# Performance work log

Measured on AMD Instinct MI355X. Metric: run time of the kernel, lower is better.

The kernel has to match this reference:

```python
import jax, jax.numpy as jnp
import numpy as np

K, B, T, EH, DH, F = 32, 256, 32, 128, 128, 1


def _p(key, shape, scale=0.1):
    return scale * jax.random.normal(key, shape, jnp.float32)


def setup_inputs() -> dict:
    key = jax.random.key(0)
    ks = jax.random.split(key, 24)
    inp = {
        'input_encoded': jax.random.normal(ks[0], (B, T, EH), jnp.float32),
        'y_prev': jax.random.normal(ks[1], (B, T), jnp.float32),
        'eps': jax.random.normal(ks[2], (T, K, B, DH), jnp.float32),
        'gumbel': jax.random.gumbel(ks[3], (T, B, K, K), jnp.float32),
        # attn_layer: Linear(2*DH+EH -> EH), Tanh, Linear(EH -> 1)
        'attn_W1': _p(ks[4], (2 * DH + EH, EH)),
        'attn_b1': _p(ks[5], (EH,)),
        'attn_W2': _p(ks[6], (EH, 1)),
        'attn_b2': _p(ks[7], (1,)),
        # LSTM(input_size=F, hidden_size=DH); gate order i,f,g,o
        'W_ih': _p(ks[8], (F, 4 * DH)),
        'W_hh': _p(ks[9], (DH, 4 * DH)),
        'b_ih': _p(ks[10], (4 * DH,)),
        'b_hh': _p(ks[11], (4 * DH,)),
        # fc: Linear(EH+F -> F), weights initialized normal_() in torch
        'fc_W': jax.random.normal(ks[12], (EH + F, F), jnp.float32),
        'fc_b': _p(ks[13], (F,)),
        # fc_decoder_final: Linear(DH -> F)
        'fcdec_W': _p(ks[14], (DH, F)),
        'fcdec_b': _p(ks[15], (F,)),
        # fc_encoder_final (passed-in module, modeled as Linear(EH -> F))
        'fcenc_W': _p(ks[16], (EH, F)),
        'fcenc_b': _p(ks[17], (F,)),
        # var_layer: Linear(DH+F -> DH); pdf_layer: Linear(DH+F -> 1)
        'var_W': _p(ks[18], (DH + F, DH)),
        'var_b': _p(ks[19], (DH,)),
        'pdf_W': _p(ks[20], (DH + F, 1)),
        'pdf_b': _p(ks[21], (1,)),
    }
    return inp


def _decoder_fwd(input_encoded, y_prev, eps, gumbel, attn_W1, attn_b1, attn_W2,
                 attn_b2, W_ih, W_hh, b_ih, b_hh, fc_W, fc_b, fcdec_W, fcdec_b,
                 fcenc_W, fcenc_b, var_W, var_b, pdf_W, pdf_b):
    Bn, Tn, EHn = input_encoded.shape
    Kn = eps.shape[1]
    DHn = W_hh.shape[0]

    def lstm_cell(x, h, c):  # x:[N,F], h/c:[N,DH]
        g = x @ W_ih + h @ W_hh + (b_ih + b_hh)
        i, f, gg, o = jnp.split(g, 4, axis=-1)
        c2 = jax.nn.sigmoid(f) * c + jax.nn.sigmoid(i) * jnp.tanh(gg)
        h2 = jax.nn.sigmoid(o) * jnp.tanh(c2)
        return h2, c2

    def step(carry, inp):
        hiddens, cells, _ = carry          # [K,B,DH] particle-major
        yprev_t, eps_t, g_t = inp          # [B], [K,B,DH], [B,K,K]
        hbar = hiddens.mean(axis=0)        # [B,DH]
        cbar = cells.mean(axis=0)
        # attention over all T encoder states
        x = jnp.concatenate([
            jnp.broadcast_to(hbar[:, None, :], (Bn, Tn, DHn)),
            jnp.broadcast_to(cbar[:, None, :], (Bn, Tn, DHn)),
            input_encoded], axis=2)                       # [B,T,2DH+EH]
        a = jnp.tanh(x @ attn_W1 + attn_b1) @ attn_W2 + attn_b2  # [B,T,1]
        beta = jax.nn.softmax(a[..., 0], axis=1)                 # [B,T]
        context = jnp.einsum('bt,bte->be', beta, input_encoded)  # [B,EH]
        y_tilde = jnp.concatenate([context, yprev_t[:, None]], axis=1) @ fc_W + fc_b  # [B,F]
        var = jnp.concatenate([y_tilde, hbar], axis=1) @ var_W + var_b  # [B,DH]
        # one LSTM step for all particles (same input, per-particle state)
        xin = jnp.broadcast_to(y_tilde[None], (Kn, Bn, y_tilde.shape[1])).reshape(Kn * Bn, -1)
        h2, c2 = lstm_cell(xin, hiddens.reshape(Kn * Bn, DHn), cells.reshape(Kn * Bn, DHn))
        h2 = h2.reshape(Kn, Bn, DHn)
        c2 = c2.reshape(Kn, Bn, DHn)
        # reparameterize: mu + eps * softplus(var)
        h2 = h2 + eps_t * jax.nn.softplus(var)[None]
        # sort particles per batch by scalar projection (only hiddens sorted)
        proj = (h2.reshape(-1, DHn) @ fcdec_W + fcdec_b).reshape(Kn, Bn)  # [K,B]
        order = jnp.argsort(proj, axis=0)                                  # [K,B]
        h2 = jnp.take_along_axis(h2, order[:, :, None], axis=0)
        # particle weights; replicate torch's view(-1, K) normalization exactly
        y = jnp.concatenate([h2.reshape(-1, DHn), jnp.tile(y_tilde, (Kn, 1))], axis=1)
        logpdf = (y @ pdf_W + pdf_b)[:, 0]          # [K*B] particle-major flat
        p = jnp.exp(logpdf).reshape(Bn, Kn)         # torch view(-1, K, 1)
        p = p / p.sum(axis=1, keepdims=True)
        w = p.reshape(Kn, Bn).T                     # [B,K]: torch view(K,-1).T
        # multinomial with replacement via gumbel-max (row-normalization implicit)
        idx = jnp.argmax(jnp.log(w + 1e-30)[:, None, :] + g_t, axis=-1)  # [B,K]
        sel = idx.T                                  # [K,B]: new[p,b] = old[idx[b,p], b]
        h2 = jnp.take_along_axis(h2, sel[:, :, None], axis=0)
        c2 = jnp.take_along_axis(c2, sel[:, :, None], axis=0)
        return (h2, c2, context), None

    h0 = jnp.zeros((Kn, Bn, DHn), input_encoded.dtype)
    ctx0 = jnp.zeros((Bn, EHn), input_encoded.dtype)
    (hK, cK, context), _ = jax.lax.scan(step, (h0, h0, ctx0), (y_prev.T, eps, gumbel))
    y_decoder_pred = hK.mean(axis=0) @ fcdec_W + fcdec_b   # [B,F]
    y_encoder_pred = context @ fcenc_W + fcenc_b           # [B,F]
    return y_decoder_pred + y_encoder_pred


def reference(input_encoded, y_prev, eps, gumbel, attn_W1, attn_b1, attn_W2,
              attn_b2, W_ih, W_hh, b_ih, b_hh, fc_W, fc_b, fcdec_W, fcdec_b,
              fcenc_W, fcenc_b, var_W, var_b, pdf_W, pdf_b):
    return _decoder_fwd(input_encoded, y_prev, eps, gumbel, attn_W1, attn_b1,
                        attn_W2, attn_b2, W_ih, W_hh, b_ih, b_hh, fc_W, fc_b,
                        fcdec_W, fcdec_b, fcenc_W, fcenc_b, var_W, var_b,
                        pdf_W, pdf_b)
```

## Files before the change

kernel.cpp:

```cpp
#include <hip/hip_runtime.h>

#define KP 32
#define BN 256
#define TN 32
#define ROWS (KP*BN)
#define NTHR 512

__global__ void k_pre(const float* __restrict__ enc, const float* __restrict__ W1,
                      const float* __restrict__ Whh, const float* __restrict__ Wih,
                      const float* __restrict__ bih, const float* __restrict__ bhh,
                      float* __restrict__ encp, float* __restrict__ Wre,
                      float* __restrict__ wihre, float* __restrict__ bre,
                      unsigned* __restrict__ flags) {
    int bt = blockIdx.x;
    int e  = threadIdx.x;
    __shared__ float row[128];
    row[e] = enc[bt * 128 + e];
    __syncthreads();
    float acc = 0.f;
#pragma unroll 8
    for (int c = 0; c < 128; ++c)
        acc = fmaf(row[c], W1[(256 + c) * 128 + e], acc);
    encp[bt * 128 + e] = acc;

    if (bt < 128) {
        int i = bt * 128 + e;
        int dd = i >> 7, d0 = i & 127;
        float4 v;
        v.x = Whh[dd * 512 + 0 * 128 + d0];
        v.y = Whh[dd * 512 + 1 * 128 + d0];
        v.z = Whh[dd * 512 + 2 * 128 + d0];
        v.w = Whh[dd * 512 + 3 * 128 + d0];
        ((float4*)Wre)[i] = v;
        if (i < 128) {
            float4 a;
            a.x = Wih[0 * 128 + d0]; a.y = Wih[1 * 128 + d0];
            a.z = Wih[2 * 128 + d0]; a.w = Wih[3 * 128 + d0];
            ((float4*)wihre)[d0] = a;
            float4 bb;
            bb.x = bih[0 * 128 + d0] + bhh[0 * 128 + d0];
            bb.y = bih[1 * 128 + d0] + bhh[1 * 128 + d0];
            bb.z = bih[2 * 128 + d0] + bhh[2 * 128 + d0];
            bb.w = bih[3 * 128 + d0] + bhh[3 * 128 + d0];
            ((float4*)bre)[d0] = bb;
        }
    } else if (bt < 192) {
        flags[(bt - 128) * 128 + e] = 0u;
    }
}

struct SharedS {
    float h[KP * 128], c[KP * 128], h2[KP * 128], c2[KP * 128];
    float hb[128], cb[128], hcp[128], red[128];
    float aa[32], beta[32];
    float vsp[128], ctx[128];
    float proj[32], qv[32];
    float pp[32][2], qq[32][2];
    int ord[32], hjo[32], cjo[32];
    float lw[32];
    float yts;
};

__global__ __launch_bounds__(NTHR, 2)
void k_persist(const float* __restrict__ enc, const float* __restrict__ yprev,
               const float* __restrict__ eps, const float* __restrict__ gum,
               const float* __restrict__ W1, const float* __restrict__ b1,
               const float* __restrict__ W2, const float* __restrict__ b2v,
               const float* __restrict__ fcW, const float* __restrict__ fcb,
               const float* __restrict__ fdW, const float* __restrict__ fdb,
               const float* __restrict__ feW, const float* __restrict__ feb,
               const float* __restrict__ varW, const float* __restrict__ varb,
               const float* __restrict__ pdW, const float* __restrict__ pdb,
               const float* __restrict__ encp, const float* __restrict__ Wre,
               const float* __restrict__ wihre, const float* __restrict__ bre,
               float* __restrict__ esg, unsigned* __restrict__ flags,
               float* __restrict__ out) {
    __shared__ SharedS sh;
    const int tid = threadIdx.x;
    const int b   = blockIdx.x;
    const int m   = b >> 5;

    const int w_  = tid >> 6, c0_ = tid & 63;
    const int wr_ = w_ & 3, dh_ = w_ >> 2;
    const int d0_ = dh_ * 64 + c0_;

#pragma unroll
    for (int i = 0; i < 2; ++i) {
        ((float4*)sh.h)[tid + NTHR * i] = make_float4(0.f, 0.f, 0.f, 0.f);
        ((float4*)sh.c)[tid + NTHR * i] = make_float4(0.f, 0.f, 0.f, 0.f);
    }
    __syncthreads();

    for (int t = 0; t < TN; ++t) {
        float epr[8];
        {
            const float* ep = eps + (size_t)t * ROWS * 128
                            + (size_t)(wr_ * 8) * BN * 128 + (size_t)b * 128 + d0_;
#pragma unroll
            for (int r = 0; r < 8; ++r)
                epr[r] = ep[(size_t)r * BN * 128];
        }

        {
            if (tid < 128) {
                float s = 0.f;
#pragma unroll 4
                for (int k = 0; k < KP; ++k) s += sh.h[k * 128 + tid];
                sh.hb[tid] = s * (1.f / 32.f);
            } else if (tid < 256) {
                int d = tid - 128;
                float s = 0.f;
#pragma unroll 4
                for (int k = 0; k < KP; ++k) s += sh.c[k * 128 + d];
                sh.cb[d] = s * (1.f / 32.f);
            }
            __syncthreads();

            float acc2 = 0.f;
            {
                int e = tid & 127, half = (tid >> 7) & 1;
                if (tid < 256) {
                    const float* Wb  = W1 + half * 128 * 128;
                    const float* hcl = half ? sh.cb : sh.hb;
#pragma unroll 8
                    for (int d = 0; d < 128; ++d)
                        acc2 = fmaf(hcl[d], Wb[d * 128 + e], acc2);
                    if (half) sh.red[e] = acc2;
                }
            }
            __syncthreads();
            if (tid < 128) sh.hcp[tid] = acc2 + sh.red[tid] + b1[tid];
            __syncthreads();

            if (tid < 256) {
                int w = tid >> 6, lane = tid & 63;
                for (int tt = 0; tt < 8; ++tt) {
                    int tq = w * 8 + tt;
                    float v = 0.f;
#pragma unroll
                    for (int hh = 0; hh < 2; ++hh) {
                        int e = lane + 64 * hh;
                        v += tanhf(sh.hcp[e] + encp[(b * TN + tq) * 128 + e]) * W2[e];
                    }
#pragma unroll
                    for (int off = 32; off; off >>= 1) v += __shfl_xor(v, off, 64);
                    if (lane == 0) sh.aa[tq] = v + b2v[0];
                }
            }
            __syncthreads();

            if (tid < 32) {
                float mx = -1e30f;
                for (int i = 0; i < 32; ++i) mx = fmaxf(mx, sh.aa[i]);
                float s = 0.f;
                for (int i = 0; i < 32; ++i) s += expf(sh.aa[i] - mx);
                sh.beta[tid] = expf(sh.aa[tid] - mx) / s;
            }
            __syncthreads();

            if (tid < 128) {
                float acc = 0.f;
#pragma unroll 4
                for (int tq = 0; tq < 32; ++tq)
                    acc = fmaf(sh.beta[tq], enc[(b * TN + tq) * 128 + tid], acc);
                sh.ctx[tid] = acc;
                sh.red[tid] = acc * fcW[tid];
            }
            __syncthreads();
            if (tid < 64) sh.red[tid] += sh.red[tid + 64];
            __syncthreads();
            if (tid < 64) {
                float v = sh.red[tid];
#pragma unroll
                for (int off = 32; off; off >>= 1) v += __shfl_xor(v, off, 64);
                if (tid == 0)
                    sh.yts = v + yprev[b * TN + t] * fcW[128] + fcb[0];
            }
            __syncthreads();

            if (tid < 128) {
                int j = tid;
                float v = fmaf(sh.yts, varW[j], varb[j]);
#pragma unroll 8
                for (int d = 0; d < 128; ++d)
                    v = fmaf(sh.hb[d], varW[(1 + d) * 128 + j], v);
                sh.vsp[j] = fmaxf(v, 0.f) + log1pf(expf(-fabsf(v)));
            }
        }
        __syncthreads();

        {
            float4 wih4 = ((const float4*)wihre)[d0_];
            float4 b4   = ((const float4*)bre)[d0_];
            const float* wihp = (const float*)&wih4;
            const float* bp   = (const float*)&b4;
            float ytv = sh.yts;
            float acc[8][4];
#pragma unroll
            for (int r = 0; r < 8; ++r)
#pragma unroll
                for (int g = 0; g < 4; ++g)
                    acc[r][g] = fmaf(ytv, wihp[g], bp[g]);

            const float4* wp   = (const float4*)Wre + d0_;
            const float*  hrow = sh.h + (wr_ * 8) * 128;
#pragma unroll 2
            for (int dq = 0; dq < 32; ++dq) {
                float4 wv[4];
#pragma unroll
                for (int j = 0; j < 4; ++j) wv[j] = wp[(dq * 4 + j) * 128];
                float4 hv[8];
#pragma unroll
                for (int r = 0; r < 8; ++r)
                    hv[r] = *(const float4*)&hrow[r * 128 + dq * 4];
#pragma unroll
                for (int j = 0; j < 4; ++j) {
#pragma unroll
                    for (int r = 0; r < 8; ++r) {
                        float hvj = ((const float*)&hv[r])[j];
#pragma unroll
                        for (int g = 0; g < 4; ++g)
                            acc[r][g] = fmaf(hvj, ((const float*)&wv[j])[g], acc[r][g]);
                    }
                }
            }

            float fdv = fdW[d0_], pdv = pdW[d0_];
#pragma unroll
            for (int r = 0; r < 8; ++r) {
                int lr = wr_ * 8 + r;
                float gi = acc[r][0], gf = acc[r][1], gg = acc[r][2], go = acc[r][3];
                float si = 1.f / (1.f + expf(-gi));
                float sf = 1.f / (1.f + expf(-gf));
                float so = 1.f / (1.f + expf(-go));
                float tg = tanhf(gg);
                float cold = sh.c[lr * 128 + d0_];
                float cnv = sf * cold + si * tg;
                float hnv = so * tanhf(cnv);
                hnv = fmaf(epr[r], sh.vsp[d0_], hnv);
                sh.c2[lr * 128 + d0_] = cnv;
                sh.h2[lr * 128 + d0_] = hnv;
                float p = hnv * fdv, q = hnv * pdv;
#pragma unroll
                for (int off = 32; off; off >>= 1) {
                    p += __shfl_xor(p, off, 64);
                    q += __shfl_xor(q, off, 64);
                }
                if (c0_ == 0) { sh.pp[lr][dh_] = p; sh.qq[lr][dh_] = q; }
            }
            __syncthreads();
            if (tid < 32) sh.proj[tid] = sh.pp[tid][0] + sh.pp[tid][1];
            else if (tid < 64) sh.qv[tid - 32] = sh.qq[tid - 32][0] + sh.qq[tid - 32][1];
        }
        __syncthreads();

        if (tid < 32) {
            int j = tid;
            float pj = sh.proj[j];
            int r = 0;
#pragma unroll 8
            for (int l = 0; l < 32; ++l) {
                float pl = sh.proj[l];
                r += (pl < pj) || (pl == pj && l < j);
            }
            sh.ord[r] = j;
        }
        __syncthreads();
        float esj = 0.f;
        if (tid < 32) {
            int j = tid;
            int jo = sh.ord[j];
            float lp = sh.qv[jo] + sh.yts * pdW[128] + pdb[0];
            esj = expf(lp);
            esg[(size_t)(t & 1) * (BN * KP) + b * KP + j] = esj;
            __builtin_amdgcn_fence(__ATOMIC_RELEASE, "agent");
            if (j == 0)
                __hip_atomic_store(&flags[b * 32], (unsigned)(t + 1),
                                   __ATOMIC_RELAXED, __HIP_MEMORY_SCOPE_AGENT);
            while (__hip_atomic_load(&flags[(m * 32 + j) * 32],
                                     __ATOMIC_RELAXED, __HIP_MEMORY_SCOPE_AGENT)
                   < (unsigned)(t + 1))
                __builtin_amdgcn_s_sleep(2);
        }
        __syncthreads();
        asm volatile("" ::: "memory");
        if (tid < 32) {
            int j = tid;
            const float* eb = esg + (size_t)(t & 1) * (BN * KP) + (m * 32) * KP + j;
            float S = 0.f;
#pragma unroll 8
            for (int l = 0; l < 32; ++l)
                S += __hip_atomic_load(&eb[l * KP], __ATOMIC_RELAXED, __HIP_MEMORY_SCOPE_AGENT);
            sh.lw[j] = logf(esj / S + 1e-30f);
        }
        __syncthreads();
        if (tid < 32) {
            int j = tid;
            const float* gb = gum + (((size_t)t * BN + b) * KP + j) * KP;
            float best = -1e38f;
            int bi = 0;
#pragma unroll 8
            for (int l = 0; l < 32; ++l) {
                float v = sh.lw[l] + gb[l];
                if (v > best) { best = v; bi = l; }
            }
            sh.hjo[j] = sh.ord[bi];
            sh.cjo[j] = bi;
        }
        __syncthreads();
#pragma unroll
        for (int it = 0; it < 2; ++it) {
            int i = tid + NTHR * it;
            int r = i >> 5, o = i & 31;
            ((float4*)sh.h)[i] = ((float4*)sh.h2)[sh.hjo[r] * 32 + o];
            ((float4*)sh.c)[i] = ((float4*)sh.c2)[sh.cjo[r] * 32 + o];
        }
        __syncthreads();
    }

    if (tid < 64) {
        int lane = tid;
        float acc = 0.f;
#pragma unroll
        for (int hh = 0; hh < 2; ++hh) {
            int d = lane + 64 * hh;
            float s = 0.f;
#pragma unroll 4
            for (int k = 0; k < KP; ++k) s += sh.h[k * 128 + d];
            acc = fmaf(s * (1.f / 32.f), fdW[d], acc);
            acc = fmaf(sh.ctx[d], feW[d], acc);
        }
#pragma unroll
        for (int off = 32; off; off >>= 1) acc += __shfl_xor(acc, off, 64);
        if (lane == 0) out[b] = acc + fdb[0] + feb[0];
    }
}

extern "C" void kernel_launch(void* const* d_in, const int* in_sizes, int n_in,
                              void* d_out, int out_size, void* d_ws, size_t ws_size,
                              hipStream_t stream) {
    const float* enc   = (const float*)d_in[0];
    const float* yprev = (const float*)d_in[1];
    const float* eps   = (const float*)d_in[2];
    const float* gum   = (const float*)d_in[3];
    const float* aW1   = (const float*)d_in[4];
    const float* ab1   = (const float*)d_in[5];
    const float* aW2   = (const float*)d_in[6];
    const float* ab2   = (const float*)d_in[7];
    const float* Wih   = (const float*)d_in[8];
    const float* Whh   = (const float*)d_in[9];
    const float* bih   = (const float*)d_in[10];
    const float* bhh   = (const float*)d_in[11];
    const float* fcW   = (const float*)d_in[12];
    const float* fcb   = (const float*)d_in[13];
    const float* fdW   = (const float*)d_in[14];
    const float* fdb   = (const float*)d_in[15];
    const float* feW   = (const float*)d_in[16];
    const float* feb   = (const float*)d_in[17];
    const float* varW  = (const float*)d_in[18];
    const float* varb  = (const float*)d_in[19];
    const float* pdW   = (const float*)d_in[20];
    const float* pdb   = (const float*)d_in[21];
    float* out = (float*)d_out;

    float* ws     = (float*)d_ws;
    float* encp   = ws;
    float* Wre    = ws + 1048576;
    float* wihre  = ws + 1114112;
    float* bre    = ws + 1114624;
    float* esg    = ws + 1115136;
    unsigned* flags = (unsigned*)(ws + 1131520);

    k_pre<<<BN * TN, 128, 0, stream>>>(enc, aW1, Whh, Wih, bih, bhh,
                                       encp, Wre, wihre, bre, flags);
    k_persist<<<BN, NTHR, 0, stream>>>(enc, yprev, eps, gum, aW1, ab1, aW2, ab2,
                                       fcW, fcb, fdW, fdb, feW, feb, varW, varb,
                                       pdW, pdb, encp, Wre, wihre, bre,
                                       esg, flags, out);
}
```

Baseline: 1.672 ms.

## Double persistent block to 1024 threads and merge single-wave phases

Raises the persistent kernel's block size from 512 to 1024 threads, so each wave handles 4 particle rows instead of 8 in the LSTM gate GEMM. The attention scoring now runs across all 16 waves. The eps, h and accumulator arrays per thread shrink accordingly. Several tid<32 phases (sort rank, weight normalisation after the cross-block spin-wait, gumbel argmax) are merged into one single-wavefront section, dropping several block-wide barriers per step. This relies on LDS ordering within one wave, and the larger launch-bounds occupancy request may squeeze the register budget.

```diff
diff --git a/kernel.cpp b/kernel.cpp
--- a/kernel.cpp
+++ b/kernel.cpp
@@ -4,7 +4,7 @@
 #define BN 256
 #define TN 32
 #define ROWS (KP*BN)
-#define NTHR 512
+#define NTHR 1024
 
 __global__ void k_pre(const float* __restrict__ enc, const float* __restrict__ W1,
                       const float* __restrict__ Whh, const float* __restrict__ Wih,
@@ -61,7 +61,7 @@
     float yts;
 };
 
-__global__ __launch_bounds__(NTHR, 2)
+__global__ __launch_bounds__(NTHR, 4)
 void k_persist(const float* __restrict__ enc, const float* __restrict__ yprev,
                const float* __restrict__ eps, const float* __restrict__ gum,
                const float* __restrict__ W1, const float* __restrict__ b1,
@@ -81,23 +81,20 @@
     const int m   = b >> 5;
 
     const int w_  = tid >> 6, c0_ = tid & 63;
-    const int wr_ = w_ & 3, dh_ = w_ >> 2;
+    const int pg_ = w_ & 7, dh_ = w_ >> 3;
     const int d0_ = dh_ * 64 + c0_;
 
-#pragma unroll
-    for (int i = 0; i < 2; ++i) {
-        ((float4*)sh.h)[tid + NTHR * i] = make_float4(0.f, 0.f, 0.f, 0.f);
-        ((float4*)sh.c)[tid + NTHR * i] = make_float4(0.f, 0.f, 0.f, 0.f);
-    }
+    ((float4*)sh.h)[tid] = make_float4(0.f, 0.f, 0.f, 0.f);
+    ((float4*)sh.c)[tid] = make_float4(0.f, 0.f, 0.f, 0.f);
     __syncthreads();
 
     for (int t = 0; t < TN; ++t) {
-        float epr[8];
+        float epr[4];
         {
             const float* ep = eps + (size_t)t * ROWS * 128
-                            + (size_t)(wr_ * 8) * BN * 128 + (size_t)b * 128 + d0_;
-#pragma unroll
-            for (int r = 0; r < 8; ++r)
+                            + (size_t)(pg_ * 4) * BN * 128 + (size_t)b * 128 + d0_;
+#pragma unroll
+            for (int r = 0; r < 4; ++r)
                 epr[r] = ep[(size_t)r * BN * 128];
         }
 
@@ -132,10 +129,11 @@
             if (tid < 128) sh.hcp[tid] = acc2 + sh.red[tid] + b1[tid];
             __syncthreads();
 
-            if (tid < 256) {
-                int w = tid >> 6, lane = tid & 63;
-                for (int tt = 0; tt < 8; ++tt) {
-                    int tq = w * 8 + tt;
+            {
+                int lane = tid & 63;
+#pragma unroll
+                for (int tt = 0; tt < 2; ++tt) {
+                    int tq = w_ * 2 + tt;
                     float v = 0.f;
 #pragma unroll
                     for (int hh = 0; hh < 2; ++hh) {
@@ -167,10 +165,8 @@
                 sh.red[tid] = acc * fcW[tid];
             }
             __syncthreads();
-            if (tid < 64) sh.red[tid] += sh.red[tid + 64];
-            __syncthreads();
             if (tid < 64) {
-                float v = sh.red[tid];
+                float v = sh.red[tid] + sh.red[tid + 64];
 #pragma unroll
                 for (int off = 32; off; off >>= 1) v += __shfl_xor(v, off, 64);
                 if (tid == 0)
@@ -195,28 +191,28 @@
             const float* wihp = (const float*)&wih4;
             const float* bp   = (const float*)&b4;
             float ytv = sh.yts;
-            float acc[8][4];
-#pragma unroll
-            for (int r = 0; r < 8; ++r)
+            float acc[4][4];
+#pragma unroll
+            for (int r = 0; r < 4; ++r)
 #pragma unroll
                 for (int g = 0; g < 4; ++g)
                     acc[r][g] = fmaf(ytv, wihp[g], bp[g]);
 
             const float4* wp   = (const float4*)Wre + d0_;
-            const float*  hrow = sh.h + (wr_ * 8) * 128;
+            const float*  hrow = sh.h + (pg_ * 4) * 128;
 #pragma unroll 2
             for (int dq = 0; dq < 32; ++dq) {
                 float4 wv[4];
 #pragma unroll
                 for (int j = 0; j < 4; ++j) wv[j] = wp[(dq * 4 + j) * 128];
-                float4 hv[8];
-#pragma unroll
-                for (int r = 0; r < 8; ++r)
+                float4 hv[4];
+#pragma unroll
+                for (int r = 0; r < 4; ++r)
                     hv[r] = *(const float4*)&hrow[r * 128 + dq * 4];
 #pragma unroll
                 for (int j = 0; j < 4; ++j) {
 #pragma unroll
-                    for (int r = 0; r < 8; ++r) {
+                    for (int r = 0; r < 4; ++r) {
                         float hvj = ((const float*)&hv[r])[j];
 #pragma unroll
                         for (int g = 0; g < 4; ++g)
@@ -227,8 +223,8 @@
 
             float fdv = fdW[d0_], pdv = pdW[d0_];
 #pragma unroll
-            for (int r = 0; r < 8; ++r) {
-                int lr = wr_ * 8 + r;
+            for (int r = 0; r < 4; ++r) {
+                int lr = pg_ * 4 + r;
                 float gi = acc[r][0], gf = acc[r][1], gg = acc[r][2], go = acc[r][3];
                 float si = 1.f / (1.f + expf(-gi));
                 float sf = 1.f / (1.f + expf(-gf));
@@ -254,6 +250,7 @@
         }
         __syncthreads();
 
+        float esj = 0.f;
         if (tid < 32) {
             int j = tid;
             float pj = sh.proj[j];
@@ -264,11 +261,6 @@
                 r += (pl < pj) || (pl == pj && l < j);
             }
             sh.ord[r] = j;
-        }
-        __syncthreads();
-        float esj = 0.f;
-        if (tid < 32) {
-            int j = tid;
             int jo = sh.ord[j];
             float lp = sh.qv[jo] + sh.yts * pdW[128] + pdb[0];
             esj = expf(lp);
@@ -281,21 +273,13 @@
                                      __ATOMIC_RELAXED, __HIP_MEMORY_SCOPE_AGENT)
                    < (unsigned)(t + 1))
                 __builtin_amdgcn_s_sleep(2);
-        }
-        __syncthreads();
-        asm volatile("" ::: "memory");
-        if (tid < 32) {
-            int j = tid;
+            asm volatile("" ::: "memory");
             const float* eb = esg + (size_t)(t & 1) * (BN * KP) + (m * 32) * KP + j;
             float S = 0.f;
 #pragma unroll 8
             for (int l = 0; l < 32; ++l)
                 S += __hip_atomic_load(&eb[l * KP], __ATOMIC_RELAXED, __HIP_MEMORY_SCOPE_AGENT);
             sh.lw[j] = logf(esj / S + 1e-30f);
-        }
-        __syncthreads();
-        if (tid < 32) {
-            int j = tid;
             const float* gb = gum + (((size_t)t * BN + b) * KP + j) * KP;
             float best = -1e38f;
             int bi = 0;
@@ -308,12 +292,10 @@
             sh.cjo[j] = bi;
         }
         __syncthreads();
-#pragma unroll
-        for (int it = 0; it < 2; ++it) {
-            int i = tid + NTHR * it;
-            int r = i >> 5, o = i & 31;
-            ((float4*)sh.h)[i] = ((float4*)sh.h2)[sh.hjo[r] * 32 + o];
-            ((float4*)sh.c)[i] = ((float4*)sh.c2)[sh.cjo[r] * 32 + o];
+        {
+            int r = tid >> 5, o = tid & 31;
+            ((float4*)sh.h)[tid] = ((float4*)sh.h2)[sh.hjo[r] * 32 + o];
+            ((float4*)sh.c)[tid] = ((float4*)sh.c2)[sh.cjo[r] * 32 + o];
         }
         __syncthreads();
     }
```

Result: faster. 1.507 ms (-9.8%).
